# Optimization experiments

Hardware: AMD Instinct MI355X
Metric: run time of the kernel (lower is better)

The kernel has to match this reference:

```python
import jax, jax.numpy as jnp
import numpy as np

N_NODES = 15000
N_EDGES = 60000
D_NODE_IN = 74
D_EDGE_IN = 12
D = 64            # node_out_feats
D_EHID = 128      # edge_hidden_feats
N_STEPS = 6
BN_EPS = 1e-5


def setup_inputs() -> dict:
    key = jax.random.key(0)
    ks = jax.random.split(key, 16)
    def lin(k, fan_in, shape):
        return jax.random.normal(k, shape, jnp.float32) / np.sqrt(fan_in)
    inp = {
        "node_feats": jax.random.normal(ks[0], (N_NODES, D_NODE_IN), jnp.float32),
        "edge_feats": jax.random.normal(ks[1], (N_EDGES, D_EDGE_IN), jnp.float32),
        "src": jax.random.randint(ks[2], (N_EDGES,), 0, N_NODES, jnp.int32),
        "dst": jax.random.randint(ks[3], (N_EDGES,), 0, N_NODES, jnp.int32),
        # project_node_feats: Linear(node_in, D)
        "W_proj": lin(ks[4], D_NODE_IN, (D_NODE_IN, D)),
        "b_proj": jnp.zeros((D,), jnp.float32),
        # edge network: Linear(edge_in, ehid) -> ReLU -> Linear(ehid, D*D)
        "W_e1": lin(ks[5], D_EDGE_IN, (D_EDGE_IN, D_EHID)),
        "b_e1": jnp.zeros((D_EHID,), jnp.float32),
        "W_e2": lin(ks[6], D_EHID, (D_EHID, D * D)),
        "b_e2": jnp.zeros((D * D,), jnp.float32),
        # NNConv bias + BatchNorm affine params
        "conv_bias": jnp.zeros((D,), jnp.float32),
        "bn_gamma": jnp.ones((D,), jnp.float32),
        "bn_beta": jnp.zeros((D,), jnp.float32),
        # GRU (single layer): torch layout W_ih [3D, D], W_hh [3D, D]
        "W_ih": lin(ks[7], D, (3 * D, D)),
        "W_hh": lin(ks[8], D, (3 * D, D)),
        "b_ih": jnp.zeros((3 * D,), jnp.float32),
        "b_hh": jnp.zeros((3 * D,), jnp.float32),
    }
    return inp


def reference(node_feats, edge_feats, W_proj, b_proj, W_e1, b_e1, W_e2, b_e2,
              conv_bias, bn_gamma, bn_beta, W_ih, W_hh, b_ih, b_hh, src, dst):
    n_nodes = node_feats.shape[0]

    # project_node_feats: Linear + ReLU
    h = jax.nn.relu(node_feats @ W_proj + b_proj)          # [N, D]
    hidden = h                                              # GRU hidden state

    # edge MLP is a pure function of static edge_feats -> compute once
    ew = jax.nn.relu(edge_feats @ W_e1 + b_e1) @ W_e2 + b_e2
    ew = ew.reshape(-1, D, D)                               # [E, D, D]

    # mean-aggregation normalizer (DGL mean: 0 for isolated nodes)
    deg = jax.ops.segment_sum(jnp.ones_like(dst, jnp.float32), dst,
                              num_segments=n_nodes)
    inv_deg = jnp.where(deg > 0, 1.0 / jnp.maximum(deg, 1.0), 0.0)[:, None]

    for _ in range(N_STEPS):
        # per-edge matvec message: (h_src^T W_e); sum over d_in commutes
        # with the mean reduction, so reduce vectors instead of matrices.
        msg = jnp.einsum('ei,eio->eo', h[src], ew)          # [E, D]
        rst = jax.ops.segment_sum(msg, dst, num_segments=n_nodes) * inv_deg
        rst = rst + conv_bias
        # BatchNorm1d (training mode: batch statistics, biased variance)
        mu = rst.mean(axis=0)
        var = rst.var(axis=0)
        rst = (rst - mu) * jax.lax.rsqrt(var + BN_EPS) * bn_gamma + bn_beta
        m = jax.nn.relu(rst)
        # GRU cell (torch gate order: r, z, n)
        gi = m @ W_ih.T + b_ih
        gh = hidden @ W_hh.T + b_hh
        i_r, i_z, i_n = jnp.split(gi, 3, axis=-1)
        h_r, h_z, h_n = jnp.split(gh, 3, axis=-1)
        r = jax.nn.sigmoid(i_r + h_r)
        z = jax.nn.sigmoid(i_z + h_z)
        n = jnp.tanh(i_n + r * h_n)
        hidden = (1.0 - z) * n + z * hidden
        h = hidden
    return h
```

## Files before the change

### kernel.cpp

```cpp
#include <hip/hip_runtime.h>
#include <hip/hip_bf16.h>
#include <math.h>

#define NN 15000
#define NE 60000
#define DIN 74
#define DEIN 12
#define DD 64
#define EH 128
#define NG 8192
#define NSTEPS 6
#define NRB 235
#define NGB 235
#define KAB 384
#define NTMAX 18752
#define NFB 586

typedef unsigned short ushort_t;
typedef __attribute__((ext_vector_type(8))) short short8v;
typedef __attribute__((ext_vector_type(4))) float float4v;

__device__ __forceinline__ float bsf(unsigned short u){
  union { unsigned int i; float f; } v; v.i = ((unsigned int)u) << 16; return v.f;
}
__device__ __forceinline__ unsigned short fsb(float f){
  union { float f; unsigned int i; } v; v.f = f;
  unsigned int x = v.i;
  return (unsigned short)((x + 0x7FFFu + ((x >> 16) & 1u)) >> 16);
}
__device__ __forceinline__ unsigned int pkbf(float a, float b){
  __hip_bfloat162 r = __float22bfloat162_rn(make_float2(a, b));
  union { __hip_bfloat162 h; unsigned int u; } v; v.h = r; return v.u;
}

__global__ void k_sniff(const ushort_t* __restrict__ nf16,
                        const int* __restrict__ dsti, int* __restrict__ flags){
  __shared__ int cnt[2];
  int t = threadIdx.x;
  if (t < 2) cnt[t] = 0;
  __syncthreads();
  int bad = 0;
  for (int i = t; i < 1024; i += 256){
    unsigned short u = nf16[2*i];
    int e = (u >> 7) & 0xFF;
    if (e < 96 || e > 159) bad++;
  }
  if (bad) atomicAdd(&cnt[0], bad);
  if (t < 256 && dsti[2*t+1] == 0) atomicAdd(&cnt[1], 1);
  __syncthreads();
  if (t == 0){
    flags[0] = (cnt[0] > 300) ? 1 : 0;
    flags[1] = (cnt[1] > 250) ? 1 : 0;
  }
}

struct CanonArgs {
  const void* in[15];
  float* out[15];
  int n[15];
};
__global__ void k_canon_all(CanonArgs a, const int* __restrict__ flags){
  int j = blockIdx.y;
  int n = a.n[j];
  int fp32 = flags[0];
  const void* in = a.in[j];
  float* out = a.out[j];
  for (int i = blockIdx.x*256 + threadIdx.x; i < n; i += gridDim.x*256){
    if (fp32) out[i] = ((const float*)in)[i];
    else      out[i] = bsf(((const ushort_t*)in)[i]);
  }
}
__global__ void k_canoni2(const void* __restrict__ in0, const void* __restrict__ in1,
                          int* __restrict__ out0, int* __restrict__ out1,
                          const int* __restrict__ flags){
  int i = blockIdx.x*256 + threadIdx.x;
  if (i >= NE) return;
  const void* in = blockIdx.y ? in1 : in0;
  int* out = blockIdx.y ? out1 : out0;
  long long v = flags[1] ? ((const long long*)in)[i]
                         : (long long)((const int*)in)[i];
  int vi = (int)v;
  if (vi < 0) vi = 0;
  if (vi >= NN) vi = NN-1;
  out[i] = vi;
}

__global__ void k_proj(const float* __restrict__ nf, const float* __restrict__ Wp,
                       const float* __restrict__ bp, float* __restrict__ hid,
                       ushort_t* __restrict__ ab){
  __shared__ float nfl[4][DIN];
  int t = threadIdx.x, blk = blockIdx.x;
  for (int idx = t; idx < 4*DIN; idx += 256){
    int vl = idx / DIN, i = idx - vl*DIN;
    nfl[vl][i] = nf[(size_t)(blk*4+vl)*DIN + i];
  }
  __syncthreads();
  int vl = t >> 6, o = t & 63;
  int v = blk*4 + vl;
  float acc = bp[o];
  for (int i = 0; i < DIN; ++i) acc += nfl[vl][i] * Wp[i*DD + o];
  float r = fmaxf(acc, 0.f);
  hid[(size_t)v*DD + o] = r;
  ushort_t hh = fsb(r);
  float hl = r - bsf(hh);
  ab[(size_t)v*KAB + 64 + o]  = hh;
  ab[(size_t)v*KAB + 192 + o] = fsb(hl);
  ab[(size_t)v*KAB + 320 + o] = hh;
}

__global__ void k_emlp(const float* __restrict__ ef, const float* __restrict__ W1,
                       const float* __restrict__ b1, ushort_t* __restrict__ thi,
                       ushort_t* __restrict__ tlo){
  __shared__ float efl[2][DEIN];
  int t = threadIdx.x, blk = blockIdx.x;
  if (t < 2*DEIN){
    int el = t / DEIN, i = t - el*DEIN;
    efl[el][i] = ef[(size_t)(blk*2+el)*DEIN + i];
  }
  __syncthreads();
  int el = t >> 7, c = t & 127;
  float acc = b1[c];
  for (int i = 0; i < DEIN; ++i) acc += efl[el][i] * W1[i*EH + c];
  float tv = fmaxf(acc, 0.f);
  ushort_t hiv = fsb(tv);
  size_t off = (size_t)(blk*2+el)*EH + c;
  thi[off] = hiv;
  tlo[off] = fsb(tv - bsf(hiv));
}
__global__ void k_zpad(ushort_t* __restrict__ thi, ushort_t* __restrict__ tlo){
  int t = threadIdx.x;
  thi[(size_t)NE*EH + t] = 0;
  tlo[(size_t)NE*EH + t] = 0;
}

__global__ void k_w2q(const float* __restrict__ W2, const float* __restrict__ b2,
                      ushort_t* __restrict__ w2q, ushort_t* __restrict__ w2b){
  int idx = blockIdx.x*256 + threadIdx.x;
  if (idx < NG*DD){
    int n = idx >> 6, i = idx & 63;
    int kq = n >> 11, rem = n & 2047;
    int o = rem >> 5, kl = rem & 31;
    int kg = kq*32 + kl;
    w2q[idx] = fsb(W2[(size_t)kg*4096 + i*64 + o]);
  } else if (idx < NG*DD + DD*DD){
    int r = idx - NG*DD;
    int o = r >> 6, i = r & 63;
    w2b[r] = fsb(b2[i*64 + o]);
  }
}

__global__ void k_wgru(const float* __restrict__ Wih, const float* __restrict__ Whh,
                       ushort_t* __restrict__ wg){
  int pos = blockIdx.x*256 + threadIdx.x;
  if (pos >= 256*KAB) return;
  int c = pos / KAB, k = pos - c*KAB;
  int kb = k >> 6, i = k & 63;
  int g = c >> 6, o = c & 63;
  float w = 0.f;
  if ((kb & 1) == 0){
    if (g == 0)      w = Wih[(size_t)(o)*64 + i];
    else if (g == 1) w = Wih[(size_t)(64+o)*64 + i];
    else if (g == 2) w = Wih[(size_t)(128+o)*64 + i];
  } else {
    if (g == 0)      w = Whh[(size_t)(o)*64 + i];
    else if (g == 1) w = Whh[(size_t)(64+o)*64 + i];
    else if (g == 3) w = Whh[(size_t)(128+o)*64 + i];
  }
  ushort_t hi = fsb(w);
  wg[pos] = (kb >= 4) ? fsb(w - bsf(hi)) : hi;
}

__global__ void k_zero(int* __restrict__ p, int n){
  int i = blockIdx.x*256 + threadIdx.x;
  if (i < n) p[i] = 0;
}
__global__ void k_deg2(const int* __restrict__ a0, const int* __restrict__ a1,
                       int* __restrict__ d0, int* __restrict__ d1){
  int e = blockIdx.x*256 + threadIdx.x;
  if (e < NE){
    if (blockIdx.y == 0) atomicAdd(&d0[a0[e]], 1);
    else                 atomicAdd(&d1[a1[e]], 1);
  }
}
__global__ void k_scan2(const int* __restrict__ degA, int* __restrict__ rowpA,
                        float* __restrict__ invdA,
                        const int* __restrict__ degB, int* __restrict__ rowpB,
                        float* __restrict__ invdB){
  const int* deg = blockIdx.x ? degB : degA;
  int* rowp      = blockIdx.x ? rowpB : rowpA;
  float* invd    = blockIdx.x ? invdB : invdA;
  __shared__ int ssum[256];
  int t = threadIdx.x;
  const int STRIP = (NN + 255) / 256;
  int lo = t*STRIP, hi = (lo + STRIP < NN) ? lo + STRIP : NN;
  int s = 0;
  for (int i = lo; i < hi; ++i) s += deg[i];
  ssum[t] = s;
  __syncthreads();
  if (t == 0){
    int acc = 0;
    for (int i = 0; i < 256; ++i){ int v = ssum[i]; ssum[i] = acc; acc += v; }
  }
  __syncthreads();
  int acc = ssum[t];
  for (int i = lo; i < hi; ++i){
    rowp[i] = acc;
    int d = deg[i];
    invd[i] = (d > 0) ? 1.0f/(float)d : 0.0f;
    acc += d;
  }
  if (t == 255) rowp[NN] = acc;
}
__global__ void k_scatter2(const int* __restrict__ dstc, const int* __restrict__ rowpD,
                           int* __restrict__ curD, int* __restrict__ eidxD,
                           int* __restrict__ epos,
                           const int* __restrict__ srcc, const int* __restrict__ rowpS,
                           int* __restrict__ curS, int* __restrict__ eidxS){
  int e = blockIdx.x*256 + threadIdx.x;
  if (e >= NE) return;
  if (blockIdx.y == 0){
    int d = dstc[e];
    int pos = atomicAdd(&curD[d], 1);
    int slot = rowpD[d] + pos;
    eidxD[slot] = e;
    epos[e] = slot;
  } else {
    int d = srcc[e];
    int pos = atomicAdd(&curS[d], 1);
    eidxS[rowpS[d] + pos] = e;
  }
}

__global__ void k_tiles(const int* __restrict__ rowp, int* __restrict__ tnode,
                        int* __restrict__ tbase, int* __restrict__ tcnt,
                        int* __restrict__ ntb){
  __shared__ int ss[256];
  int t = threadIdx.x;
  const int STRIP = (NN + 255) / 256;
  int lo = t*STRIP, hi = lo + STRIP; if (hi > NN) hi = NN;
  int c = 0;
  for (int i = lo; i < hi; ++i){
    int deg = rowp[i+1] - rowp[i];
    c += (deg + 15) >> 4;
  }
  ss[t] = c;
  __syncthreads();
  if (t == 0){
    int a = 0;
    for (int i = 0; i < 256; ++i){ int v = ss[i]; ss[i] = a; a += v; }
    ntb[0] = a;
  }
  __syncthreads();
  int pos = ss[t];
  for (int i = lo; i < hi; ++i){
    int b = rowp[i], deg = rowp[i+1] - b;
    for (int r = 0; r < deg; r += 16){
      tnode[pos] = i; tbase[pos] = b + r;
      int c2 = deg - r; tcnt[pos] = (c2 > 16) ? 16 : c2;
      ++pos;
    }
  }
}

__global__ __launch_bounds__(512,4) void k_fused7(
    const ushort_t* __restrict__ ab, const ushort_t* __restrict__ w2q,
    const ushort_t* __restrict__ w2b, const ushort_t* __restrict__ thi,
    const ushort_t* __restrict__ tlo,
    const int* __restrict__ tnode, const int* __restrict__ tbase,
    const int* __restrict__ tcnt, const int* __restrict__ ntb,
    const int* __restrict__ eidx, const int* __restrict__ epos,
    float* __restrict__ msg){
  __shared__ __align__(16) ushort_t Gl[32768];
  __shared__ float bhl[32*66];
  __shared__ int nodl[32], cntl[32], basel[32];
  __shared__ int eidl[32][16];
  __shared__ int posl[32][16];

  int tid = threadIdx.x;
  int nt = ntb[0];
  int T0 = blockIdx.x * 32;
  if (T0 >= nt) return;
  int wv = tid >> 6, lane = tid & 63;
  int lr = lane & 15, quad = lane >> 4;

  if (tid < 32){
    int gt = T0 + tid;
    int node = 0, base = 0, cnt = 0;
    if (gt < nt){ node = tnode[gt]; base = tbase[gt]; cnt = tcnt[gt]; }
    nodl[tid] = node; basel[tid] = base; cntl[tid] = cnt;
  }
  __syncthreads();
  {
    int j = tid >> 4, sl = tid & 15;
    int eid = NE, ps = 0;
    if (sl < cntl[j]){
      eid = eidx[basel[j] + sl];
      ps = epos[eid];
    }
    eidl[j][sl] = eid;
    posl[j][sl] = ps;
  }
  short8v hf0k0, hf0k1, hf1k0, hf1k1;
  {
    int n0 = nodl[lr], n1 = nodl[16 + lr];
    hf0k0 = *(const short8v*)(ab + (size_t)n0*KAB + 64 + quad*8);
    hf0k1 = *(const short8v*)(ab + (size_t)n0*KAB + 96 + quad*8);
    hf1k0 = *(const short8v*)(ab + (size_t)n1*KAB + 64 + quad*8);
    hf1k1 = *(const short8v*)(ab + (size_t)n1*KAB + 96 + quad*8);
  }
  {
    int ot = wv & 3, mh = wv >> 2;
    float4v ba = (float4v){0.f,0.f,0.f,0.f};
    short8v a0 = *(const short8v*)(w2b + (size_t)(ot*16 + lr)*DD + quad*8);
    short8v a1 = *(const short8v*)(w2b + (size_t)(ot*16 + lr)*DD + 32 + quad*8);
    ba = __builtin_amdgcn_mfma_f32_16x16x32_bf16(a0, mh ? hf1k0 : hf0k0, ba, 0,0,0);
    ba = __builtin_amdgcn_mfma_f32_16x16x32_bf16(a1, mh ? hf1k1 : hf0k1, ba, 0,0,0);
    #pragma unroll
    for (int reg = 0; reg < 4; ++reg)
      bhl[(mh*16 + lr)*66 + ot*16 + quad*4 + reg] = ba[reg];
  }

  int j0 = wv*4;
  for (int oh = 0; oh < 2; ++oh){
    float4v acc[4][2];
    #pragma unroll
    for (int j = 0; j < 4; ++j)
      #pragma unroll
      for (int ot = 0; ot < 2; ++ot)
        acc[j][ot] = (float4v){0.f,0.f,0.f,0.f};
    for (int kq = 0; kq < 4; ++kq){
      __syncthreads();
      #pragma unroll 4
      for (int it = 0; it < 8; ++it){
        int tile = wv*8 + it;
        int nrow = kq*2048 + oh*1024 + tile*16 + lr;
        const ushort_t* arow = w2q + (size_t)nrow*DD;
        short8v a0 = *(const short8v*)(arow + quad*8);
        short8v a1 = *(const short8v*)(arow + 32 + quad*8);
        int ol = tile >> 1;
        int klb = ((tile & 1) << 4) + quad*4;
        int q8 = klb >> 3, jj = klb & 7;
        #pragma unroll
        for (int mh = 0; mh < 2; ++mh){
          float4v g = (float4v){0.f,0.f,0.f,0.f};
          g = __builtin_amdgcn_mfma_f32_16x16x32_bf16(a0, mh ? hf1k0 : hf0k0, g, 0,0,0);
          g = __builtin_amdgcn_mfma_f32_16x16x32_bf16(a1, mh ? hf1k1 : hf0k1, g, 0,0,0);
          int m = mh*16 + lr;
          unsigned int p0 = pkbf(g[0], g[1]);
          unsigned int p1 = pkbf(g[2], g[3]);
          int byt = ((((m*4 + q8)*32 + ol) << 4) + jj*2) ^ ((m & 7) << 4);
          uint2 pv; pv.x = p0; pv.y = p1;
          *(uint2*)((char*)Gl + byt) = pv;
        }
      }
      short8v th0, th1, th2, th3, tw0, tw1, tw2, tw3;
      {
        size_t kqo = (size_t)kq*32 + quad*8;
        int e0 = eidl[j0+0][lr], e1 = eidl[j0+1][lr];
        int e2 = eidl[j0+2][lr], e3 = eidl[j0+3][lr];
        th0 = *(const short8v*)(thi + (size_t)e0*EH + kqo);
        tw0 = *(const short8v*)(tlo + (size_t)e0*EH + kqo);
        th1 = *(const short8v*)(thi + (size_t)e1*EH + kqo);
        tw1 = *(const short8v*)(tlo + (size_t)e1*EH + kqo);
        th2 = *(const short8v*)(thi + (size_t)e2*EH + kqo);
        tw2 = *(const short8v*)(tlo + (size_t)e2*EH + kqo);
        th3 = *(const short8v*)(thi + (size_t)e3*EH + kqo);
        tw3 = *(const short8v*)(tlo + (size_t)e3*EH + kqo);
      }
      __syncthreads();
      #pragma unroll
      for (int j = 0; j < 4; ++j){
        int m = j0 + j;
        int swz = (m & 7) << 4;
        short8v thj = (j==0)?th0:(j==1)?th1:(j==2)?th2:th3;
        short8v twj = (j==0)?tw0:(j==1)?tw1:(j==2)?tw2:tw3;
        #pragma unroll
        for (int ot = 0; ot < 2; ++ot){
          int byt = (((m*4 + quad)*32 + ot*16 + lr) << 4) ^ swz;
          short8v gf = *(const short8v*)((const char*)Gl + byt);
          acc[j][ot] = __builtin_amdgcn_mfma_f32_16x16x32_bf16(thj, gf, acc[j][ot], 0,0,0);
          acc[j][ot] = __builtin_amdgcn_mfma_f32_16x16x32_bf16(twj, gf, acc[j][ot], 0,0,0);
        }
      }
    }
    #pragma unroll
    for (int j = 0; j < 4; ++j){
      int m = j0 + j;
      #pragma unroll
      for (int ot = 0; ot < 2; ++ot){
        int o = oh*32 + ot*16 + lr;
        float bb = bhl[m*66 + o];
        #pragma unroll
        for (int reg = 0; reg < 4; ++reg){
          int sl = quad*4 + reg;
          int eid = eidl[m][sl];
          if (eid < NE) msg[(size_t)posl[m][sl]*DD + o] = acc[j][ot][reg] + bb;
        }
      }
    }
  }
}

__global__ __launch_bounds__(512) void k_red(const float* __restrict__ msg,
                      const int* __restrict__ rowp_d,
                      const float* __restrict__ invd, const float* __restrict__ cbias,
                      float* __restrict__ rst, float* __restrict__ part){
  __shared__ float ls[512], ls2[512];
  int t = threadIdx.x, blk = blockIdx.x;
  int o = t & 63, gg = t >> 6;
  float cb = cbias[o];
  float s = 0.f, s2 = 0.f;
  #pragma unroll 1
  for (int j = 0; j < 8; ++j){
    int n = blk*64 + gg*8 + j;
    if (n >= NN) break;
    int b = rowp_d[n], e = rowp_d[n+1];
    float a0 = 0.f, a1 = 0.f, a2 = 0.f, a3 = 0.f;
    int i = b;
    for (; i + 3 < e; i += 4){
      a0 += msg[(size_t)i*DD + o];
      a1 += msg[(size_t)(i+1)*DD + o];
      a2 += msg[(size_t)(i+2)*DD + o];
      a3 += msg[(size_t)(i+3)*DD + o];
    }
    for (; i < e; ++i) a0 += msg[(size_t)i*DD + o];
    float x = ((a0 + a1) + (a2 + a3)) * invd[n] + cb;
    rst[(size_t)n*DD + o] = x;
    s += x; s2 += x*x;
  }
  ls[t] = s; ls2[t] = s2;
  __syncthreads();
  if (t < 64){
    float a = 0.f;
    #pragma unroll
    for (int g = 0; g < 8; ++g) a += ls[g*64 + t];
    part[blk*128 + t] = a;
  } else if (t < 128){
    int o2 = t - 64;
    float a = 0.f;
    #pragma unroll
    for (int g = 0; g < 8; ++g) a += ls2[g*64 + o2];
    part[blk*128 + 64 + o2] = a;
  }
}

__global__ __launch_bounds__(512) void k_gru_one(
    const float* __restrict__ rst, const float* __restrict__ part,
    const float* __restrict__ gamma, const float* __restrict__ beta,
    ushort_t* __restrict__ ab, const ushort_t* __restrict__ wg,
    const float* __restrict__ bih, const float* __restrict__ bhh,
    float* __restrict__ hid, float* __restrict__ out, int write_out){
  __shared__ __align__(16) ushort_t As[64][136];
  __shared__ __align__(16) ushort_t Bs[256][136];
  __shared__ float gl[64*257];
  __shared__ float scl[64], sft[64];
  __shared__ float sh[128];
  int t = threadIdx.x;
  int r0 = blockIdx.x * 64;
  if (t < 128){
    float s0 = 0.f, s1 = 0.f, s2 = 0.f, s3 = 0.f;
    int b = 0;
    for (; b + 3 < NRB; b += 4){
      s0 += part[b*128 + t];
      s1 += part[(b+1)*128 + t];
      s2 += part[(b+2)*128 + t];
      s3 += part[(b+3)*128 + t];
    }
    for (; b < NRB; ++b) s0 += part[b*128 + t];
    sh[t] = (s0 + s1) + (s2 + s3);
  }
  __syncthreads();
  if (t < 64){
    float mu = sh[t] / (float)NN;
    float var = sh[64+t] / (float)NN - mu*mu;
    if (var < 0.f) var = 0.f;
    float rsq = rsqrtf(var + 1e-5f);
    float sc = rsq * gamma[t];
    scl[t] = sc;
    sft[t] = beta[t] - mu*sc;
  }
  int wv = t >> 6, lane = t & 63;
  int lr = lane & 15, quad = lane >> 4;
  int n0 = wv * 32;
  float4v acc[4][2];
  #pragma unroll
  for (int mt = 0; mt < 4; ++mt)
    #pragma unroll
    for (int nt = 0; nt < 2; ++nt) acc[mt][nt] = (float4v){0.f,0.f,0.f,0.f};
  for (int kt = 0; kt < 3; ++kt){
    __syncthreads();
    #pragma unroll
    for (int it = 0; it < 2; ++it){
      int cid = t + it*512;
      int r = cid >> 4, ko = (cid & 15) * 8;
      int gm = r0 + r; if (gm >= NN) gm = NN-1;
      if (ko < 64){
        float4 x0 = *(const float4*)(rst + (size_t)gm*DD + ko);
        float4 x1 = *(const float4*)(rst + (size_t)gm*DD + ko + 4);
        float xv[8] = {x0.x,x0.y,x0.z,x0.w,x1.x,x1.y,x1.z,x1.w};
        ushort_t u[8];
        #pragma unroll
        for (int jj = 0; jj < 8; ++jj){
          float m = fmaxf(xv[jj]*scl[ko+jj] + sft[ko+jj], 0.f);
          ushort_t mh = fsb(m);
          u[jj] = (kt == 1) ? fsb(m - bsf(mh)) : mh;
        }
        *(uint4*)&As[r][ko] = *(const uint4*)u;
      } else {
        *(uint4*)&As[r][ko] = *(const uint4*)(ab + (size_t)gm*KAB + kt*128 + ko);
      }
    }
    #pragma unroll
    for (int it = 0; it < 8; ++it){
      int cid = t + it*512;
      int rB = cid >> 4, ko = (cid & 15) * 8;
      *(uint4*)&Bs[rB][ko] = *(const uint4*)(wg + (size_t)rB*KAB + kt*128 + ko);
    }
    __syncthreads();
    #pragma unroll
    for (int ks = 0; ks < 4; ++ks){
      short8v a[4];
      #pragma unroll
      for (int mt = 0; mt < 4; ++mt)
        a[mt] = *(const short8v*)&As[mt*16 + lr][ks*32 + quad*8];
      #pragma unroll
      for (int nt = 0; nt < 2; ++nt){
        short8v b = *(const short8v*)&Bs[n0 + nt*16 + lr][ks*32 + quad*8];
        #pragma unroll
        for (int mt = 0; mt < 4; ++mt)
          acc[mt][nt] = __builtin_amdgcn_mfma_f32_16x16x32_bf16(a[mt], b, acc[mt][nt], 0,0,0);
      }
    }
  }
  #pragma unroll
  for (int mt = 0; mt < 4; ++mt)
    #pragma unroll
    for (int nt = 0; nt < 2; ++nt){
      int col = n0 + nt*16 + lr;
      #pragma unroll
      for (int reg = 0; reg < 4; ++reg)
        gl[(mt*16 + quad*4 + reg)*257 + col] = acc[mt][nt][reg];
    }
  __syncthreads();
  for (int idx = t; idx < 64*64; idx += 512){
    int row = idx >> 6, o = idx & 63;
    int v = r0 + row;
    if (v >= NN) break;
    const float* g = &gl[row*257];
    float aR  = g[o]       + bih[o]      + bhh[o];
    float aZ  = g[64 + o]  + bih[64+o]   + bhh[64+o];
    float aNi = g[128 + o] + bih[128+o];
    float aNh = g[192 + o] + bhh[128+o];
    float hprev = hid[(size_t)v*DD + o];
    float r = 1.f/(1.f+__expf(-aR));
    float z = 1.f/(1.f+__expf(-aZ));
    float n = tanhf(aNi + r*aNh);
    float hnew = (1.f - z)*n + z*hprev;
    hid[(size_t)v*DD + o] = hnew;
    ushort_t hh = fsb(hnew);
    float hl = hnew - bsf(hh);
    ab[(size_t)v*KAB + 64 + o]  = hh;
    ab[(size_t)v*KAB + 192 + o] = fsb(hl);
    ab[(size_t)v*KAB + 320 + o] = hh;
    if (write_out) out[(size_t)v*DD + o] = hnew;
  }
}

extern "C" void kernel_launch(void* const* d_in, const int* in_sizes, int n_in,
                              void* d_out, int out_size, void* d_ws, size_t ws_size,
                              hipStream_t stream){
  (void)out_size; (void)ws_size;
  float* out = (float*)d_out;

  int p_nf=-1,p_ef=-1,p_src=-1,p_dst=-1,p_Wp=-1,p_bp=-1,p_W1=-1,p_b1=-1,
      p_W2=-1,p_b2=-1,p_cb=-1,p_gam=-1,p_bet=-1,p_Wih=-1,p_Whh=-1,p_bih=-1,p_bhh=-1;
  int c60000=0,c64=0,c12288=0,c192=0;
  for (int i = 0; i < n_in; ++i){
    switch (in_sizes[i]){
      case 1110000: p_nf = i; break;
      case 720000:  p_ef = i; break;
      case 60000:   if (c60000++ == 0) p_src = i; else p_dst = i; break;
      case 4736:    p_Wp = i; break;
      case 64:      { if (c64==0) p_bp=i; else if (c64==1) p_cb=i;
                      else if (c64==2) p_gam=i; else p_bet=i; c64++; } break;
      case 1536:    p_W1 = i; break;
      case 128:     p_b1 = i; break;
      case 524288:  p_W2 = i; break;
      case 4096:    p_b2 = i; break;
      case 12288:   if (c12288++ == 0) p_Wih = i; else p_Whh = i; break;
      case 192:    if (c192++ == 0) p_bih = i; else p_bhh = i; break;
      default: break;
    }
  }

  char* p = (char*)d_ws;
  auto alloc = [&](size_t bytes)->char*{
    char* r = p; p += (bytes + 255) & ~(size_t)255; return r;
  };
  int* flags = (int*)alloc(256);
  const int FPOS[15] = {p_nf,p_ef,p_Wp,p_bp,p_W1,p_b1,p_W2,p_b2,p_cb,p_gam,p_bet,
                        p_Wih,p_Whh,p_bih,p_bhh};
  CanonArgs ca;
  int maxn = 0;
  for (int j = 0; j < 15; ++j){
    int n = in_sizes[FPOS[j]];
    ca.in[j]  = d_in[FPOS[j]];
    ca.out[j] = (float*)alloc((size_t)n * 4);
    ca.n[j]   = n;
    if (n > maxn) maxn = n;
  }
  const float* nf  = ca.out[0];  const float* ef  = ca.out[1];
  const float* Wp  = ca.out[2];  const float* bp  = ca.out[3];
  const float* W1  = ca.out[4];  const float* b1  = ca.out[5];
  const float* W2  = ca.out[6];  const float* b2  = ca.out[7];
  const float* cb  = ca.out[8];  const float* gam = ca.out[9];
  const float* bet = ca.out[10]; const float* Wih = ca.out[11];
  const float* Whh = ca.out[12]; const float* bih = ca.out[13];
  const float* bhh = ca.out[14];
  int* srcc = (int*)alloc((size_t)NE*4);
  int* dstc = (int*)alloc((size_t)NE*4);

  ushort_t* thi   = (ushort_t*)alloc((size_t)(NE+1)*EH*2);
  ushort_t* tlo   = (ushort_t*)alloc((size_t)(NE+1)*EH*2);
  ushort_t* w2q   = (ushort_t*)alloc((size_t)NG*DD*2);
  ushort_t* w2b   = (ushort_t*)alloc((size_t)DD*DD*2);
  float* hid      = (float*)alloc((size_t)NN*DD*4);
  ushort_t* ab    = (ushort_t*)alloc((size_t)NN*KAB*2);
  ushort_t* wg    = (ushort_t*)alloc((size_t)256*KAB*2);
  float* rst      = (float*)alloc((size_t)NN*DD*4);
  float* msg      = (float*)alloc((size_t)NE*DD*4);
  float* part     = (float*)alloc((size_t)NRB*128*4);
  int* degall     = (int*)alloc((size_t)4*NN*4);
  int* deg  = degall;
  int* curd = degall + NN;
  int* deg2 = degall + 2*NN; int* cursor2 = degall + 3*NN;
  float* invd = (float*)alloc((size_t)NN*4);
  int* rowp_d = (int*)alloc((size_t)(NN+1)*4);
  int* eidx_d = (int*)alloc((size_t)NE*4);
  int* epos   = (int*)alloc((size_t)NE*4);
  int* rowp2  = (int*)alloc((size_t)(NN+1)*4);
  float* invd2= (float*)alloc((size_t)NN*4);
  int* eidx2  = (int*)alloc((size_t)NE*4);
  int* tnode  = (int*)alloc((size_t)NTMAX*4);
  int* tbase  = (int*)alloc((size_t)NTMAX*4);
  int* tcnt   = (int*)alloc((size_t)NTMAX*4);
  int* ntb    = (int*)alloc(256);

  k_sniff<<<1, 256, 0, stream>>>((const ushort_t*)d_in[p_nf], (const int*)d_in[p_dst], flags);
  k_canon_all<<<dim3((maxn+255)/256, 15), 256, 0, stream>>>(ca, flags);
  k_canoni2<<<dim3((NE+255)/256, 2), 256, 0, stream>>>(d_in[p_src], d_in[p_dst],
                                                       srcc, dstc, flags);

  k_proj <<<NN/4,  256, 0, stream>>>(nf, Wp, bp, hid, ab);
  k_emlp <<<NE/2,  256, 0, stream>>>(ef, W1, b1, thi, tlo);
  k_zpad <<<1, 128, 0, stream>>>(thi, tlo);
  k_w2q  <<<(NG*DD + DD*DD + 255)/256, 256, 0, stream>>>(W2, b2, w2q, w2b);
  k_wgru <<<(256*KAB+255)/256, 256, 0, stream>>>(Wih, Whh, wg);
  k_zero <<<(4*NN+255)/256, 256, 0, stream>>>(degall, 4*NN);
  k_deg2 <<<dim3((NE+255)/256, 2), 256, 0, stream>>>(dstc, srcc, deg, deg2);
  k_scan2<<<2, 256, 0, stream>>>(deg, rowp_d, invd, deg2, rowp2, invd2);
  k_scatter2<<<dim3((NE+255)/256, 2), 256, 0, stream>>>(dstc, rowp_d, curd, eidx_d,
                                                        epos, srcc, rowp2, cursor2, eidx2);
  k_tiles<<<1, 256, 0, stream>>>(rowp2, tnode, tbase, tcnt, ntb);

  for (int s = 0; s < NSTEPS; ++s){
    k_fused7<<<NFB, 512, 0, stream>>>(ab, w2q, w2b, thi, tlo,
                                      tnode, tbase, tcnt, ntb, eidx2, epos, msg);
    k_red <<<NRB, 512, 0, stream>>>(msg, rowp_d, invd, cb, rst, part);
    k_gru_one<<<NGB, 512, 0, stream>>>(rst, part, gam, bet, ab, wg, bih, bhh,
                                       hid, out, (s == NSTEPS-1) ? 1 : 0);
  }
}
```

Measured before the change: 944.2 us.

## Double-buffer shared G tile and software-pipeline the two GEMM stages

Rewrites the fused message kernel so the shared-memory G buffer is double-buffered (128KB). It fully unrolls the eight (oh,kq) chunks into a software pipeline where GEMM1 for chunk c+1 and the edge-feature loads overlap GEMM2 for chunk c. This halves the barriers per chunk and keeps all 64 output columns in registers, so results are written once. In exchange, occupancy drops to 2 blocks per CU (launch bounds 512,2) and register pressure rises with 16 accumulators and two sets of prefetched operands.

After: 979.1 us. 3.7% more time.

```diff
diff --git a/kernel.cpp b/kernel.cpp
--- a/kernel.cpp
+++ b/kernel.cpp
@@ -262,7 +262,59 @@
   }
 }
 
-__global__ __launch_bounds__(512,4) void k_fused7(
+#define LOADT(TH, TW, c) do{                                                  \
+    size_t kqo_ = (size_t)((c) & 3)*32 + quad*8;                              \
+    _Pragma("unroll")                                                         \
+    for (int j_ = 0; j_ < 4; ++j_){                                           \
+      TH[j_] = *(const short8v*)(thi + (size_t)ej[j_]*EH + kqo_);             \
+      TW[j_] = *(const short8v*)(tlo + (size_t)ej[j_]*EH + kqo_);             \
+    }                                                                         \
+  }while(0)
+
+#define GEMM1(c, B) do{                                                       \
+    const int oh_ = (c) >> 2, kq_ = (c) & 3;                                  \
+    _Pragma("unroll")                                                         \
+    for (int it_ = 0; it_ < 8; ++it_){                                        \
+      int tile_ = wv*8 + it_;                                                 \
+      int nrow_ = kq_*2048 + oh_*1024 + tile_*16 + lr;                        \
+      const ushort_t* arow_ = w2q + (size_t)nrow_*DD;                         \
+      short8v a0_ = *(const short8v*)(arow_ + quad*8);                        \
+      short8v a1_ = *(const short8v*)(arow_ + 32 + quad*8);                   \
+      int ol_ = tile_ >> 1;                                                   \
+      int klb_ = ((tile_ & 1) << 4) + quad*4;                                 \
+      int q8_ = klb_ >> 3, jj_ = klb_ & 7;                                    \
+      _Pragma("unroll")                                                       \
+      for (int mh_ = 0; mh_ < 2; ++mh_){                                      \
+        float4v g_ = (float4v){0.f,0.f,0.f,0.f};                              \
+        g_ = __builtin_amdgcn_mfma_f32_16x16x32_bf16(a0_, mh_ ? hf1k0 : hf0k0, g_, 0,0,0); \
+        g_ = __builtin_amdgcn_mfma_f32_16x16x32_bf16(a1_, mh_ ? hf1k1 : hf0k1, g_, 0,0,0); \
+        int m_ = mh_*16 + lr;                                                 \
+        unsigned int p0_ = pkbf(g_[0], g_[1]);                                \
+        unsigned int p1_ = pkbf(g_[2], g_[3]);                                \
+        int byt_ = ((((m_*4 + q8_)*32 + ol_) << 4) + jj_*2) ^ ((m_ & 7) << 4);\
+        uint2 pv_; pv_.x = p0_; pv_.y = p1_;                                  \
+        *(uint2*)((char*)Gl + (B)*65536 + byt_) = pv_;                        \
+      }                                                                       \
+    }                                                                         \
+  }while(0)
+
+#define GEMM2(c, B, TH, TW) do{                                               \
+    const int og0_ = ((c) >> 2) * 2;                                          \
+    _Pragma("unroll")                                                         \
+    for (int j_ = 0; j_ < 4; ++j_){                                           \
+      int m_ = j0 + j_;                                                       \
+      int swz_ = (m_ & 7) << 4;                                               \
+      _Pragma("unroll")                                                       \
+      for (int ot_ = 0; ot_ < 2; ++ot_){                                      \
+        int byt_ = (((m_*4 + quad)*32 + ot_*16 + lr) << 4) ^ swz_;            \
+        short8v gf_ = *(const short8v*)((const char*)Gl + (B)*65536 + byt_);  \
+        acc[j_][og0_+ot_] = __builtin_amdgcn_mfma_f32_16x16x32_bf16(TH[j_], gf_, acc[j_][og0_+ot_], 0,0,0); \
+        acc[j_][og0_+ot_] = __builtin_amdgcn_mfma_f32_16x16x32_bf16(TW[j_], gf_, acc[j_][og0_+ot_], 0,0,0); \
+      }                                                                       \
+    }                                                                         \
+  }while(0)
+
+__global__ __launch_bounds__(512,2) void k_fused10(
     const ushort_t* __restrict__ ab, const ushort_t* __restrict__ w2q,
     const ushort_t* __restrict__ w2b, const ushort_t* __restrict__ thi,
     const ushort_t* __restrict__ tlo,
@@ -270,7 +322,7 @@
     const int* __restrict__ tcnt, const int* __restrict__ ntb,
     const int* __restrict__ eidx, const int* __restrict__ epos,
     float* __restrict__ msg){
-  __shared__ __align__(16) ushort_t Gl[32768];
+  __shared__ __align__(16) ushort_t Gl[2*32768];
   __shared__ float bhl[32*66];
   __shared__ int nodl[32], cntl[32], basel[32];
   __shared__ int eidl[32][16];
@@ -300,6 +352,12 @@
     eidl[j][sl] = eid;
     posl[j][sl] = ps;
   }
+  __syncthreads();
+  int j0 = wv*4;
+  int ej[4];
+  #pragma unroll
+  for (int j = 0; j < 4; ++j) ej[j] = eidl[j0+j][lr];
+
   short8v hf0k0, hf0k1, hf1k0, hf1k1;
   {
     int n0 = nodl[lr], n1 = nodl[16 + lr];
@@ -320,82 +378,38 @@
       bhl[(mh*16 + lr)*66 + ot*16 + quad*4 + reg] = ba[reg];
   }
 
-  int j0 = wv*4;
-  for (int oh = 0; oh < 2; ++oh){
-    float4v acc[4][2];
-    #pragma unroll
-    for (int j = 0; j < 4; ++j)
+  float4v acc[4][4];
+  #pragma unroll
+  for (int j = 0; j < 4; ++j)
+    #pragma unroll
+    for (int og = 0; og < 4; ++og)
+      acc[j][og] = (float4v){0.f,0.f,0.f,0.f};
+
+  short8v thA[4], twA[4], thB[4], twB[4];
+  LOADT(thA, twA, 0);
+  GEMM1(0, 0);
+  __syncthreads();
+  LOADT(thB, twB, 1); GEMM1(1, 1); GEMM2(0, 0, thA, twA); __syncthreads();
+  LOADT(thA, twA, 2); GEMM1(2, 0); GEMM2(1, 1, thB, twB); __syncthreads();
+  LOADT(thB, twB, 3); GEMM1(3, 1); GEMM2(2, 0, thA, twA); __syncthreads();
+  LOADT(thA, twA, 4); GEMM1(4, 0); GEMM2(3, 1, thB, twB); __syncthreads();
+  LOADT(thB, twB, 5); GEMM1(5, 1); GEMM2(4, 0, thA, twA); __syncthreads();
+  LOADT(thA, twA, 6); GEMM1(6, 0); GEMM2(5, 1, thB, twB); __syncthreads();
+  LOADT(thB, twB, 7); GEMM1(7, 1); GEMM2(6, 0, thA, twA); __syncthreads();
+  GEMM2(7, 1, thB, twB);
+
+  #pragma unroll
+  for (int j = 0; j < 4; ++j){
+    int m = j0 + j;
+    #pragma unroll
+    for (int og = 0; og < 4; ++og){
+      int o = og*16 + lr;
+      float bb = bhl[m*66 + o];
       #pragma unroll
-      for (int ot = 0; ot < 2; ++ot)
-        acc[j][ot] = (float4v){0.f,0.f,0.f,0.f};
-    for (int kq = 0; kq < 4; ++kq){
-      __syncthreads();
-      #pragma unroll 4
-      for (int it = 0; it < 8; ++it){
-        int tile = wv*8 + it;
-        int nrow = kq*2048 + oh*1024 + tile*16 + lr;
-        const ushort_t* arow = w2q + (size_t)nrow*DD;
-        short8v a0 = *(const short8v*)(arow + quad*8);
-        short8v a1 = *(const short8v*)(arow + 32 + quad*8);
-        int ol = tile >> 1;
-        int klb = ((tile & 1) << 4) + quad*4;
-        int q8 = klb >> 3, jj = klb & 7;
-        #pragma unroll
-        for (int mh = 0; mh < 2; ++mh){
-          float4v g = (float4v){0.f,0.f,0.f,0.f};
-          g = __builtin_amdgcn_mfma_f32_16x16x32_bf16(a0, mh ? hf1k0 : hf0k0, g, 0,0,0);
-          g = __builtin_amdgcn_mfma_f32_16x16x32_bf16(a1, mh ? hf1k1 : hf0k1, g, 0,0,0);
-          int m = mh*16 + lr;
-          unsigned int p0 = pkbf(g[0], g[1]);
-          unsigned int p1 = pkbf(g[2], g[3]);
-          int byt = ((((m*4 + q8)*32 + ol) << 4) + jj*2) ^ ((m & 7) << 4);
-          uint2 pv; pv.x = p0; pv.y = p1;
-          *(uint2*)((char*)Gl + byt) = pv;
-        }
-      }
-      short8v th0, th1, th2, th3, tw0, tw1, tw2, tw3;
-      {
-        size_t kqo = (size_t)kq*32 + quad*8;
-        int e0 = eidl[j0+0][lr], e1 = eidl[j0+1][lr];
-        int e2 = eidl[j0+2][lr], e3 = eidl[j0+3][lr];
-        th0 = *(const short8v*)(thi + (size_t)e0*EH + kqo);
-        tw0 = *(const short8v*)(tlo + (size_t)e0*EH + kqo);
-        th1 = *(const short8v*)(thi + (size_t)e1*EH + kqo);
-        tw1 = *(const short8v*)(tlo + (size_t)e1*EH + kqo);
-        th2 = *(const short8v*)(thi + (size_t)e2*EH + kqo);
-        tw2 = *(const short8v*)(tlo + (size_t)e2*EH + kqo);
-        th3 = *(const short8v*)(thi + (size_t)e3*EH + kqo);
-        tw3 = *(const short8v*)(tlo + (size_t)e3*EH + kqo);
-      }
-      __syncthreads();
-      #pragma unroll
-      for (int j = 0; j < 4; ++j){
-        int m = j0 + j;
-        int swz = (m & 7) << 4;
-        short8v thj = (j==0)?th0:(j==1)?th1:(j==2)?th2:th3;
-        short8v twj = (j==0)?tw0:(j==1)?tw1:(j==2)?tw2:tw3;
-        #pragma unroll
-        for (int ot = 0; ot < 2; ++ot){
-          int byt = (((m*4 + quad)*32 + ot*16 + lr) << 4) ^ swz;
-          short8v gf = *(const short8v*)((const char*)Gl + byt);
-          acc[j][ot] = __builtin_amdgcn_mfma_f32_16x16x32_bf16(thj, gf, acc[j][ot], 0,0,0);
-          acc[j][ot] = __builtin_amdgcn_mfma_f32_16x16x32_bf16(twj, gf, acc[j][ot], 0,0,0);
-        }
-      }
-    }
-    #pragma unroll
-    for (int j = 0; j < 4; ++j){
-      int m = j0 + j;
-      #pragma unroll
-      for (int ot = 0; ot < 2; ++ot){
-        int o = oh*32 + ot*16 + lr;
-        float bb = bhl[m*66 + o];
-        #pragma unroll
-        for (int reg = 0; reg < 4; ++reg){
-          int sl = quad*4 + reg;
-          int eid = eidl[m][sl];
-          if (eid < NE) msg[(size_t)posl[m][sl]*DD + o] = acc[j][ot][reg] + bb;
-        }
+      for (int reg = 0; reg < 4; ++reg){
+        int sl = quad*4 + reg;
+        int eid = eidl[m][sl];
+        if (eid < NE) msg[(size_t)posl[m][sl]*DD + o] = acc[j][og][reg] + bb;
       }
     }
   }
@@ -664,8 +678,8 @@
   k_tiles<<<1, 256, 0, stream>>>(rowp2, tnode, tbase, tcnt, ntb);
 
   for (int s = 0; s < NSTEPS; ++s){
-    k_fused7<<<NFB, 512, 0, stream>>>(ab, w2q, w2b, thi, tlo,
-                                      tnode, tbase, tcnt, ntb, eidx2, epos, msg);
+    k_fused10<<<NFB, 512, 0, stream>>>(ab, w2q, w2b, thi, tlo,
+                                       tnode, tbase, tcnt, ntb, eidx2, epos, msg);
     k_red <<<NRB, 512, 0, stream>>>(msg, rowp_d, invd, cb, rst, part);
     k_gru_one<<<NGB, 512, 0, stream>>>(rst, part, gam, bet, ab, wg, bih, bhh,
                                        hid, out, (s == NSTEPS-1) ? 1 : 0);
```
